# Kernel tuning notes

Hardware: AMD Instinct MI355X
Metric: run time of the kernel (lower is better)

## Reference

```python
import jax, jax.numpy as jnp
import numpy as np

B, S, D, E, T = 16, 128, 128, 64, 128  # batch, seq_len, token_dim, dep_dim, transformed_dim (T==D required by mask broadcast)
V_TOK, V_DEP = 100000, 64
DEPTH = 2


def setup_inputs() -> dict:
    key = jax.random.key(0)
    ks = jax.random.split(key, 12)
    return {
        "token_table": jax.random.normal(ks[0], (V_TOK, D), jnp.float32) * 0.1,
        "dep_table": jax.random.normal(ks[1], (V_DEP, E), jnp.float32) * 0.1,
        # Bilinear(D, E, T): weight [T, D, E], bias [T]
        "W1": jax.random.normal(ks[2], (T, D, E), jnp.float32) * 0.05,
        "b1": jax.random.normal(ks[3], (T,), jnp.float32) * 0.05,
        # Bilinear(D, T, D): weight [D, D, T], bias [D]
        "W2": jax.random.normal(ks[4], (D, D, T), jnp.float32) * 0.05,
        "b2": jax.random.normal(ks[5], (D,), jnp.float32) * 0.05,
        # Linear(S, 1): weight [S] (flattened [1,S]), bias [1]
        "wr": jax.random.normal(ks[6], (S,), jnp.float32) * 0.05,
        "br": jax.random.normal(ks[7], (1,), jnp.float32) * 0.05,
        "tokens": jax.random.randint(ks[8], (B, S), 0, V_TOK),
        "dep_types": jax.random.randint(ks[9], (B, S), 0, V_DEP),
        "dep_heads": jax.random.randint(ks[10], (B, S), 0, S),
    }


def _block(tok, dep_emb, heads, W1, b1, W2, b2, wr, br):
    # tok: [B,S,D], dep_emb: [B,S,E], heads: [B,S] with values in [0,S)
    b, s, d = tok.shape
    # dep_transform (Bilinear) + mask + tanh. Masked structure: full tensor
    # tde_full[b,i,j,:] = tde[b,j,:] if heads[b,j]==i else 0 (heads<S always here),
    # and tanh(0)=0, so only the i==heads[b,j] rows are nonzero after activation.
    tde = jnp.tanh(jnp.einsum('bsd,tde,bse->bst', tok, W1, dep_emb) + b1)  # [B,S,T]
    # composition bilinear at the nonzero (i==head) positions
    c_nz = jnp.tanh(jnp.einsum('bsd,pdt,bst->bsp', tok, W2, tde) + b2)    # [B,S,D]
    # at masked positions tde_full==0 -> composition output is tanh(bias)
    c_bg = jnp.tanh(b2)                                                   # [D]
    # reduction Linear(S,1): out[b,i,:] = sum_j wr[j]*c[b,i,j,:] + br
    base = jnp.sum(wr) * c_bg + br                                        # [D]
    delta = wr[None, :, None] * (c_nz - c_bg)                             # [B,S,D]
    seg = (jnp.arange(b)[:, None] * s + heads).reshape(-1)                # scatter target i=heads[b,j]
    scat = jax.ops.segment_sum(delta.reshape(b * s, d), seg, num_segments=b * s)
    return base + scat.reshape(b, s, d)


def reference(token_table, dep_table, W1, b1, W2, b2, wr, br, tokens, dep_types, dep_heads):
    tok = token_table[tokens]          # [B,S,D]
    dep = dep_table[dep_types]         # [B,S,E]
    for _ in range(DEPTH):
        tok = _block(tok, dep, dep_heads, W1, b1, W2, b2, wr, br)
    out_mask = (dep_heads == 0)[..., None].astype(tok.dtype)  # keep only root tokens
    return tok * out_mask
```

## Files before the change

### kernel.cpp

```cpp
#include <hip/hip_runtime.h>
#include <hip/hip_bf16.h>

#define BB 16
#define SS 128
#define DD 128
#define EE 64
#define TT 128
#define NN (BB*SS)
#define KSPLIT 16

typedef __attribute__((ext_vector_type(8))) short short8;
typedef __attribute__((ext_vector_type(4))) float f32x4;
typedef __attribute__((ext_vector_type(4))) unsigned int u32x4;

__device__ inline unsigned pkbf16(float a, float b) {
    unsigned r;
    asm volatile("v_cvt_pk_bf16_f32 %0, %1, %2" : "=v"(r) : "v"(a), "v"(b));
    return r;
}
__device__ inline float bflo(unsigned u) { return __builtin_bit_cast(float, (unsigned)(u << 16)); }
__device__ inline float bfhi(unsigned u) { return __builtin_bit_cast(float, (unsigned)(u & 0xffff0000u)); }

#define LDS_SWZ(row, bcol) ((row) * 256 + ((bcol) ^ (((row) & 7) << 4)))

__global__ __launch_bounds__(256) void k_prep1(const float* __restrict__ W1,
                                               const float* __restrict__ dep_table,
                                               const float* __restrict__ W2,
                                               const float* __restrict__ b2,
                                               const float* __restrict__ wr,
                                               const float* __restrict__ br,
                                               __hip_bfloat16* __restrict__ G1,
                                               __hip_bfloat16* __restrict__ W2b,
                                               float* __restrict__ basics) {
    int bid = blockIdx.x;
    int tid = threadIdx.x;
    if (bid < 512) {
        int bx = bid & 63, by = bid >> 6;
        int td = bx * 256 + tid;
        int v0 = by * 8;
        const float* w1row = W1 + (size_t)td * 64;
        float acc[8] = {};
#pragma unroll
        for (int e0 = 0; e0 < 64; e0 += 8) {
            f32x4 wa = *(const f32x4*)(w1row + e0);
            f32x4 wb = *(const f32x4*)(w1row + e0 + 4);
#pragma unroll
            for (int v = 0; v < 8; v++) {
                const float* dr = dep_table + (v0 + v) * 64 + e0;
                acc[v] += wa[0] * dr[0] + wa[1] * dr[1] + wa[2] * dr[2] + wa[3] * dr[3]
                        + wb[0] * dr[4] + wb[1] * dr[5] + wb[2] * dr[6] + wb[3] * dr[7];
            }
        }
#pragma unroll
        for (int v = 0; v < 8; v++)
            G1[(size_t)(v0 + v) * (TT * DD) + td] = __float2bfloat16(acc[v]);
    } else if (bid < 1536) {
        int cid = (bid - 512) * 256 + tid;
        int d = cid >> 11;
        int rem = cid & 2047;
        int p = rem >> 4;
        int sp = rem & 15;
        int h = sp >> 3, s = sp & 7;
        int t0 = h * 64 + ((s ^ (p & 7))) * 8;
        const float* src = W2 + ((size_t)p * 128 + d) * 128 + t0;
        f32x4 a = *(const f32x4*)(src);
        f32x4 b = *(const f32x4*)(src + 4);
        u32x4 o;
        o[0] = pkbf16(a[0], a[1]);
        o[1] = pkbf16(a[2], a[3]);
        o[2] = pkbf16(b[0], b[1]);
        o[3] = pkbf16(b[2], b[3]);
        *(u32x4*)((char*)W2b + (size_t)cid * 16) = o;
    } else {
        __shared__ float red[128];
        int t = tid;
        if (t < 128) red[t] = wr[t];
        __syncthreads();
        for (int s = 64; s > 0; s >>= 1) {
            if (t < s) red[t] += red[t + s];
            __syncthreads();
        }
        if (t < 128) {
            float swr = red[0];
            float cbg = tanhf(b2[t]);
            basics[t] = cbg;
            basics[128 + t] = swr * cbg + br[0];
        }
    }
}

__global__ __launch_bounds__(256) void k_prep2(const float* __restrict__ token_table,
                                               const int* __restrict__ tokens,
                                               const int* __restrict__ dep_types,
                                               const float* __restrict__ b1,
                                               const __hip_bfloat16* __restrict__ G1,
                                               float* __restrict__ tok,
                                               float* __restrict__ tde) {
    __shared__ float rows[2][128];
    int tid = threadIdx.x;
    int gid = blockIdx.x * 256 + tid;
    int n = gid >> 7, t = tid & 127, half = tid >> 7;
    float val = token_table[(size_t)tokens[n] * 128 + t];
    tok[gid] = val;
    rows[half][t] = val;
    __syncthreads();
    int v = dep_types[n];
    const unsigned* g = (const unsigned*)(G1 + (size_t)v * (TT * DD) + t * 128);
    const float* row = rows[half];
    float acc = b1[t];
#pragma unroll
    for (int i = 0; i < 16; i++) {
        u32x4 w = *(const u32x4*)(g + i * 4);
        acc += row[i * 8 + 0] * bflo(w[0]) + row[i * 8 + 1] * bfhi(w[0]);
        acc += row[i * 8 + 2] * bflo(w[1]) + row[i * 8 + 3] * bfhi(w[1]);
        acc += row[i * 8 + 4] * bflo(w[2]) + row[i * 8 + 5] * bfhi(w[2]);
        acc += row[i * 8 + 6] * bflo(w[3]) + row[i * 8 + 7] * bfhi(w[3]);
    }
    tde[(size_t)n * 128 + t] = tanhf(acc);
}

__global__ __launch_bounds__(256) void k_gemm(const float* __restrict__ tok,
                                              const float* __restrict__ tde,
                                              const __hip_bfloat16* __restrict__ W2b,
                                              float* __restrict__ part) {
    __shared__ char As[16384];
    __shared__ char Bs[32768];
    int nb = blockIdx.x, ks = blockIdx.y;
    int tid = threadIdx.x;
    int lane = tid & 63, w = tid >> 6;
    int wm = w >> 1, wp = w & 1;
    int n0 = nb * 64, d0 = ks * 8;
    int lrow = lane & 15, lk = lane >> 4;
    int r = tid >> 2, q = tid & 3;

    f32x4 acc[2][4] = {};

    for (int dd = 0; dd < 8; dd++) {
        int d = d0 + dd;
        const char* bsrc = (const char*)W2b + (size_t)d * 32768;
#pragma unroll
        for (int i = 0; i < 8; i++) {
            int off = (i * 256 + tid) * 16;
            *(u32x4*)(Bs + off) = *(const u32x4*)(bsrc + off);
        }
        float tokv = tok[(size_t)(n0 + r) * 128 + d];
        const float* trow = tde + (size_t)(n0 + r) * 128 + q * 32;
#pragma unroll
        for (int s = 0; s < 4; s++) {
            f32x4 x = *(const f32x4*)(trow + s * 8);
            f32x4 y = *(const f32x4*)(trow + s * 8 + 4);
            u32x4 val;
            val[0] = pkbf16(x[0] * tokv, x[1] * tokv);
            val[1] = pkbf16(x[2] * tokv, x[3] * tokv);
            val[2] = pkbf16(y[0] * tokv, y[1] * tokv);
            val[3] = pkbf16(y[2] * tokv, y[3] * tokv);
            int bcol = q * 64 + s * 16;
            *(u32x4*)(As + LDS_SWZ(r, bcol)) = val;
        }
        __syncthreads();
#pragma unroll
        for (int kk = 0; kk < 4; kk++) {
            short8 aF[2], bF[4];
#pragma unroll
            for (int mi = 0; mi < 2; mi++) {
                int row = wm * 32 + mi * 16 + lrow;
                aF[mi] = *(const short8*)(As + LDS_SWZ(row, kk * 64 + lk * 16));
            }
#pragma unroll
            for (int pj = 0; pj < 4; pj++) {
                int row = wp * 64 + pj * 16 + lrow;
                bF[pj] = *(const short8*)(Bs + LDS_SWZ(row, kk * 64 + lk * 16));
            }
#pragma unroll
            for (int mi = 0; mi < 2; mi++)
#pragma unroll
                for (int pj = 0; pj < 4; pj++)
                    acc[mi][pj] = __builtin_amdgcn_mfma_f32_16x16x32_bf16(
                        aF[mi], bF[pj], acc[mi][pj], 0, 0, 0);
        }
        __syncthreads();
    }
    float* pout = part + (size_t)ks * NN * 128;
#pragma unroll
    for (int mi = 0; mi < 2; mi++)
#pragma unroll
        for (int pj = 0; pj < 4; pj++)
#pragma unroll
            for (int rr = 0; rr < 4; rr++) {
                int row = wm * 32 + mi * 16 + (lane >> 4) * 4 + rr;
                int col = wp * 64 + pj * 16 + (lane & 15);
                pout[(size_t)(n0 + row) * 128 + col] = acc[mi][pj][rr];
            }
}

__global__ void k_e2a(const float* __restrict__ part, const int* __restrict__ heads,
                      const float* __restrict__ basics, const float* __restrict__ wr,
                      const float* __restrict__ b2, const int* __restrict__ dep_types,
                      const float* __restrict__ b1, const __hip_bfloat16* __restrict__ G1,
                      float* __restrict__ tok, float* __restrict__ tde) {
    int bi = blockIdx.x;
    int b = bi >> 7, i = bi & 127;
    int p = threadIdx.x;
    __shared__ int hs[128];
    __shared__ float row[128];
    hs[p] = heads[b * 128 + p];
    __syncthreads();
    float cbg = basics[p];
    float acc = basics[128 + p];
    for (int j = 0; j < 128; j++) {
        if (hs[j] == i) {
            int gg = (b * 128 + j) * 128 + p;
            float s = 0.f;
#pragma unroll
            for (int k = 0; k < KSPLIT; k++) s += part[(size_t)k * NN * 128 + gg];
            float c = tanhf(s + b2[p]);
            acc += wr[j] * (c - cbg);
        }
    }
    tok[(size_t)bi * 128 + p] = acc;
    row[p] = acc;
    __syncthreads();
    int v = dep_types[bi];
    const unsigned* g = (const unsigned*)(G1 + (size_t)v * (TT * DD) + p * 128);
    float a2 = b1[p];
#pragma unroll
    for (int ii = 0; ii < 16; ii++) {
        u32x4 w = *(const u32x4*)(g + ii * 4);
        a2 += row[ii * 8 + 0] * bflo(w[0]) + row[ii * 8 + 1] * bfhi(w[0]);
        a2 += row[ii * 8 + 2] * bflo(w[1]) + row[ii * 8 + 3] * bfhi(w[1]);
        a2 += row[ii * 8 + 4] * bflo(w[2]) + row[ii * 8 + 5] * bfhi(w[2]);
        a2 += row[ii * 8 + 6] * bflo(w[3]) + row[ii * 8 + 7] * bfhi(w[3]);
    }
    tde[(size_t)bi * 128 + p] = tanhf(a2);
}

__global__ void k_e2b(const float* __restrict__ part, const int* __restrict__ heads,
                      const float* __restrict__ basics, const float* __restrict__ wr,
                      const float* __restrict__ b2, float* __restrict__ out) {
    int bi = blockIdx.x;
    int b = bi >> 7, i = bi & 127;
    int p = threadIdx.x;
    __shared__ int hs[128];
    hs[p] = heads[b * 128 + p];
    __syncthreads();
    if (hs[i] != 0) {
        out[(size_t)bi * 128 + p] = 0.f;
        return;
    }
    float cbg = basics[p];
    float acc = basics[128 + p];
    for (int j = 0; j < 128; j++) {
        if (hs[j] == i) {
            int gg = (b * 128 + j) * 128 + p;
            float s = 0.f;
#pragma unroll
            for (int k = 0; k < KSPLIT; k++) s += part[(size_t)k * NN * 128 + gg];
            float c = tanhf(s + b2[p]);
            acc += wr[j] * (c - cbg);
        }
    }
    out[(size_t)bi * 128 + p] = acc;
}

extern "C" void kernel_launch(void* const* d_in, const int* in_sizes, int n_in,
                              void* d_out, int out_size, void* d_ws, size_t ws_size,
                              hipStream_t stream) {
    const float* token_table = (const float*)d_in[0];
    const float* dep_table   = (const float*)d_in[1];
    const float* W1          = (const float*)d_in[2];
    const float* b1          = (const float*)d_in[3];
    const float* W2          = (const float*)d_in[4];
    const float* b2          = (const float*)d_in[5];
    const float* wr          = (const float*)d_in[6];
    const float* br          = (const float*)d_in[7];
    const int* tokens        = (const int*)d_in[8];
    const int* dep_types     = (const int*)d_in[9];
    const int* dep_heads     = (const int*)d_in[10];
    float* out = (float*)d_out;

    char* ws = (char*)d_ws;
    __hip_bfloat16* G1  = (__hip_bfloat16*)(ws);
    __hip_bfloat16* W2b = (__hip_bfloat16*)(ws + (2ull << 20));
    float* tok    = (float*)(ws + (6ull << 20));
    float* tde    = (float*)(ws + (7ull << 20));
    float* part   = (float*)(ws + (9ull << 20));
    float* basics = (float*)(ws + (25ull << 20));

    k_prep1<<<1537, 256, 0, stream>>>(W1, dep_table, W2, b2, wr, br, G1, W2b, basics);
    k_prep2<<<1024, 256, 0, stream>>>(token_table, tokens, dep_types, b1, G1, tok, tde);

    k_gemm<<<dim3(32, KSPLIT), 256, 0, stream>>>(tok, tde, W2b, part);
    k_e2a<<<NN, 128, 0, stream>>>(part, dep_heads, basics, wr, b2,
                                  dep_types, b1, G1, tok, tde);
    k_gemm<<<dim3(32, KSPLIT), 256, 0, stream>>>(tok, tde, W2b, part);
    k_e2b<<<NN, 128, 0, stream>>>(part, dep_heads, basics, wr, b2, out);
}
```

Before: 116.7 us.

## Halve GEMM row tile to double blocks and load W2 via direct-to-LDS

The composition GEMM tile shrinks from 64 to 32 rows per block, the grid doubles from 32x16 to 64x16 blocks, and each wave now owns a 32-column slice of the output. The W2 slice is loaded with global_load_lds straight into shared memory instead of through registers, and launch bounds request 4 blocks per SM. The intent is more parallelism and occupancy and less register staging. The cost is that each W2 slice is fetched by twice as many blocks, doubling that global traffic.

```diff
diff --git a/kernel.cpp b/kernel.cpp
--- a/kernel.cpp
+++ b/kernel.cpp
@@ -119,62 +119,63 @@
     tde[(size_t)n * 128 + t] = tanhf(acc);
 }
 
-__global__ __launch_bounds__(256) void k_gemm(const float* __restrict__ tok,
-                                              const float* __restrict__ tde,
-                                              const __hip_bfloat16* __restrict__ W2b,
-                                              float* __restrict__ part) {
-    __shared__ char As[16384];
+__global__ __launch_bounds__(256, 4) void k_gemm(const float* __restrict__ tok,
+                                                 const float* __restrict__ tde,
+                                                 const __hip_bfloat16* __restrict__ W2b,
+                                                 float* __restrict__ part) {
+    __shared__ char As[8192];
     __shared__ char Bs[32768];
     int nb = blockIdx.x, ks = blockIdx.y;
     int tid = threadIdx.x;
     int lane = tid & 63, w = tid >> 6;
-    int wm = w >> 1, wp = w & 1;
-    int n0 = nb * 64, d0 = ks * 8;
+    int n0 = nb * 32, d0 = ks * 8;
     int lrow = lane & 15, lk = lane >> 4;
-    int r = tid >> 2, q = tid & 3;
-
-    f32x4 acc[2][4] = {};
+    int r = tid >> 3, o = tid & 7;
+    int wbase16 = (tid & 192) * 16;
+
+    f32x4 acc[2][2] = {};
 
     for (int dd = 0; dd < 8; dd++) {
         int d = d0 + dd;
         const char* bsrc = (const char*)W2b + (size_t)d * 32768;
 #pragma unroll
         for (int i = 0; i < 8; i++) {
-            int off = (i * 256 + tid) * 16;
-            *(u32x4*)(Bs + off) = *(const u32x4*)(bsrc + off);
+            __builtin_amdgcn_global_load_lds(
+                (const __attribute__((address_space(1))) void*)(bsrc + (i * 256 + tid) * 16),
+                (__attribute__((address_space(3))) void*)(Bs + i * 4096 + wbase16),
+                16, 0, 0);
         }
         float tokv = tok[(size_t)(n0 + r) * 128 + d];
-        const float* trow = tde + (size_t)(n0 + r) * 128 + q * 32;
-#pragma unroll
-        for (int s = 0; s < 4; s++) {
-            f32x4 x = *(const f32x4*)(trow + s * 8);
-            f32x4 y = *(const f32x4*)(trow + s * 8 + 4);
-            u32x4 val;
-            val[0] = pkbf16(x[0] * tokv, x[1] * tokv);
-            val[1] = pkbf16(x[2] * tokv, x[3] * tokv);
-            val[2] = pkbf16(y[0] * tokv, y[1] * tokv);
-            val[3] = pkbf16(y[2] * tokv, y[3] * tokv);
-            int bcol = q * 64 + s * 16;
-            *(u32x4*)(As + LDS_SWZ(r, bcol)) = val;
-        }
+        const float* trow = tde + (size_t)(n0 + r) * 128 + o * 16;
+        f32x4 xa = *(const f32x4*)(trow);
+        f32x4 xb = *(const f32x4*)(trow + 4);
+        f32x4 ya = *(const f32x4*)(trow + 8);
+        f32x4 yb = *(const f32x4*)(trow + 12);
+        u32x4 v0, v1;
+        v0[0] = pkbf16(xa[0] * tokv, xa[1] * tokv);
+        v0[1] = pkbf16(xa[2] * tokv, xa[3] * tokv);
+        v0[2] = pkbf16(xb[0] * tokv, xb[1] * tokv);
+        v0[3] = pkbf16(xb[2] * tokv, xb[3] * tokv);
+        v1[0] = pkbf16(ya[0] * tokv, ya[1] * tokv);
+        v1[1] = pkbf16(ya[2] * tokv, ya[3] * tokv);
+        v1[2] = pkbf16(yb[0] * tokv, yb[1] * tokv);
+        v1[3] = pkbf16(yb[2] * tokv, yb[3] * tokv);
+        *(u32x4*)(As + LDS_SWZ(r, o * 32))      = v0;
+        *(u32x4*)(As + LDS_SWZ(r, o * 32 + 16)) = v1;
         __syncthreads();
 #pragma unroll
         for (int kk = 0; kk < 4; kk++) {
-            short8 aF[2], bF[4];
-#pragma unroll
-            for (int mi = 0; mi < 2; mi++) {
-                int row = wm * 32 + mi * 16 + lrow;
-                aF[mi] = *(const short8*)(As + LDS_SWZ(row, kk * 64 + lk * 16));
-            }
-#pragma unroll
-            for (int pj = 0; pj < 4; pj++) {
-                int row = wp * 64 + pj * 16 + lrow;
-                bF[pj] = *(const short8*)(Bs + LDS_SWZ(row, kk * 64 + lk * 16));
-            }
+            short8 aF[2], bF[2];
 #pragma unroll
             for (int mi = 0; mi < 2; mi++)
-#pragma unroll
-                for (int pj = 0; pj < 4; pj++)
+                aF[mi] = *(const short8*)(As + LDS_SWZ(mi * 16 + lrow, kk * 64 + lk * 16));
+#pragma unroll
+            for (int pj = 0; pj < 2; pj++)
+                bF[pj] = *(const short8*)(Bs + LDS_SWZ(w * 32 + pj * 16 + lrow, kk * 64 + lk * 16));
+#pragma unroll
+            for (int mi = 0; mi < 2; mi++)
+#pragma unroll
+                for (int pj = 0; pj < 2; pj++)
                     acc[mi][pj] = __builtin_amdgcn_mfma_f32_16x16x32_bf16(
                         aF[mi], bF[pj], acc[mi][pj], 0, 0, 0);
         }
@@ -184,11 +185,11 @@
 #pragma unroll
     for (int mi = 0; mi < 2; mi++)
 #pragma unroll
-        for (int pj = 0; pj < 4; pj++)
+        for (int pj = 0; pj < 2; pj++)
 #pragma unroll
             for (int rr = 0; rr < 4; rr++) {
-                int row = wm * 32 + mi * 16 + (lane >> 4) * 4 + rr;
-                int col = wp * 64 + pj * 16 + (lane & 15);
+                int row = mi * 16 + (lane >> 4) * 4 + rr;
+                int col = w * 32 + pj * 16 + (lane & 15);
                 pout[(size_t)(n0 + row) * 128 + col] = acc[mi][pj][rr];
             }
 }
@@ -289,9 +290,9 @@
     k_prep1<<<1537, 256, 0, stream>>>(W1, dep_table, W2, b2, wr, br, G1, W2b, basics);
     k_prep2<<<1024, 256, 0, stream>>>(token_table, tokens, dep_types, b1, G1, tok, tde);
 
-    k_gemm<<<dim3(32, KSPLIT), 256, 0, stream>>>(tok, tde, W2b, part);
+    k_gemm<<<dim3(64, KSPLIT), 256, 0, stream>>>(tok, tde, W2b, part);
     k_e2a<<<NN, 128, 0, stream>>>(part, dep_heads, basics, wr, b2,
                                   dep_types, b1, G1, tok, tde);
-    k_gemm<<<dim3(32, KSPLIT), 256, 0, stream>>>(tok, tde, W2b, part);
+    k_gemm<<<dim3(64, KSPLIT), 256, 0, stream>>>(tok, tde, W2b, part);
     k_e2b<<<NN, 128, 0, stream>>>(part, dep_heads, basics, wr, b2, out);
 }
```

Measured after the change: 103.2 us. -11.6%, faster.
